# Kernel tuning notes

Hardware: AMD Instinct MI355X
Metric: run time of the kernel (lower is better)

## Reference

```python
import jax, jax.numpy as jnp
import numpy as np
import math

C = 8  # sparsity factor c from __init__


def setup_inputs() -> dict:
    key = jax.random.key(0)
    kq, kk, kv, ki = jax.random.split(key, 4)
    B, Q, KV, D = 4, 2048, 2048, 512
    U = int(Q * math.log(KV))  # 15615 sampled keys, matches torch _sampler
    q = jax.random.normal(kq, (B, Q, D), dtype=jnp.float32)
    k = jax.random.normal(kk, (B, KV, D), dtype=jnp.float32)
    v = jax.random.normal(kv, (B, KV, D), dtype=jnp.float32)
    sample_idx = jax.random.randint(ki, (B, U), 0, KV)  # per-batch random key sample
    return {"q": q, "k": k, "v": v, "sample_idx": sample_idx}


def reference(q, k, v, sample_idx):
    B, Q, D = q.shape
    KV = k.shape[1]
    u = int(C * math.log(Q))  # number of selected queries (== 60 here)

    # _sampler: gather sampled keys per batch -> (B, U, D)
    k_bar = jnp.take_along_axis(k, sample_idx[:, :, None], axis=1)

    # sparsity measure M = max_j s_bar - mean_j s_bar, s_bar: (B, Q, U)
    s_bar = jnp.einsum('bqd,bud->bqu', q, k_bar)
    M = s_bar.max(axis=2) - s_bar.mean(axis=2)  # (B, Q)

    # top-u queries per batch
    _, top_idx = jax.lax.top_k(M, u)  # (B, u)
    q_bar = jnp.take_along_axis(q, top_idx[:, :, None], axis=1)  # (B, u, D)

    # small dense attention over full keys; NOTE: original scales by sqrt(kv_len)
    attn = jnp.einsum('bud,bkd->buk', q_bar, k) / jnp.sqrt(jnp.asarray(KV, q.dtype))
    attn = jax.nn.softmax(attn, axis=-1)
    s1 = jnp.einsum('buk,bkd->bud', attn, v)  # (B, u, D)

    # fill all positions with mean of v, then scatter attention outputs
    s = jnp.broadcast_to(v.mean(axis=1, keepdims=True), q.shape)  # (B, Q, D)
    bidx = jnp.arange(B)[:, None]
    s = s.at[bidx, top_idx].set(s1)
    return s
```

## Files before the change

### kernel.cpp

```cpp
#include <hip/hip_runtime.h>
#include <math.h>

#define BATCH 4
#define QN    2048
#define KVN   2048
#define DN    512
#define U_TOT 15615
#define NSEL  60
#define NSLOT 32
#define S1KS  64

typedef __attribute__((ext_vector_type(8))) short bf16x8;
typedef __attribute__((ext_vector_type(4))) float f32x4;

__device__ __forceinline__ unsigned short f2bf(float f) {
  unsigned u = __float_as_uint(f);
  unsigned r = (u + 0x7fffu + ((u >> 16) & 1u)) >> 16;
  return (unsigned short)r;
}
__device__ __forceinline__ float bf2f(unsigned short h) {
  return __uint_as_float(((unsigned)h) << 16);
}
__device__ __forceinline__ void gld16(const void* g, void* l) {
  __builtin_amdgcn_global_load_lds(
      (const __attribute__((address_space(1))) unsigned int*)g,
      (__attribute__((address_space(3))) unsigned int*)l, 16, 0, 0);
}

__global__ __launch_bounds__(256) void split_kernel(
    const float* __restrict__ q, const float* __restrict__ k,
    unsigned short* __restrict__ qhi, unsigned short* __restrict__ qlo,
    unsigned short* __restrict__ khi, unsigned short* __restrict__ klo)
{
  const int half = blockIdx.x >> 12;
  const int i = (blockIdx.x & 4095) * 256 + threadIdx.x;
  const float* in = half ? k : q;
  unsigned short* hi = half ? khi : qhi;
  unsigned short* lo = half ? klo : qlo;
  float4 f = reinterpret_cast<const float4*>(in)[i];
  ushort4 h, l;
  h.x = f2bf(f.x); l.x = f2bf(f.x - bf2f(h.x));
  h.y = f2bf(f.y); l.y = f2bf(f.y - bf2f(h.y));
  h.z = f2bf(f.z); l.z = f2bf(f.z - bf2f(h.z));
  h.w = f2bf(f.w); l.w = f2bf(f.w - bf2f(h.w));
  reinterpret_cast<ushort4*>(hi)[i] = h;
  reinterpret_cast<ushort4*>(lo)[i] = l;
}

__global__ __launch_bounds__(1024) void count_kernel(
    const int* __restrict__ sidx, float* __restrict__ cnt)
{
  __shared__ int h[KVN];
  const int b = blockIdx.x, t = threadIdx.x;
  for (int i = t; i < KVN; i += 1024) h[i] = 0;
  __syncthreads();
  for (int i = t; i < U_TOT; i += 1024) atomicAdd(&h[sidx[b * U_TOT + i]], 1);
  __syncthreads();
  for (int i = t; i < KVN; i += 1024) cnt[b * KVN + i] = (float)h[i];
}

__global__ __launch_bounds__(256) void s_mfma_kernel(
    const unsigned short* __restrict__ qh, const unsigned short* __restrict__ ql,
    const unsigned short* __restrict__ kh, const unsigned short* __restrict__ kl,
    const float* __restrict__ cnt, float* __restrict__ Pmax, float* __restrict__ Psum)
{
  __shared__ unsigned short Ah[128 * 32];
  __shared__ unsigned short Al[128 * 32];
  __shared__ unsigned short Bh[128 * 32];
  __shared__ unsigned short Bl[128 * 32];
  __shared__ float cnt_s[128];

  const int t = threadIdx.x;
  const int w = t >> 6;
  const int L = t & 63;
  const int mbase = (w & 1) * 64;
  const int nbase = (w >> 1) * 64;
  const int lm = L & 15;

  const int bid = blockIdx.x;
  const int xcd = bid & 7;
  const int idx = bid >> 3;
  const int b   = xcd >> 1;
  const int ji  = (xcd & 1) * 8 + (idx >> 3);
  const int qi0 = (idx & 7) * 2;
  const int j0  = ji * 128;

  if (t < 128) cnt_s[t] = cnt[b * KVN + j0 + t];

  const int srow = t >> 2;
  const int schk = (t & 3) ^ ((t >> 3) & 3);

  const int perm  = (L >> 4) ^ ((lm >> 1) & 3);
  const int abase = (mbase * 4 + lm * 4 + perm) * 8;
  const int bbase = (nbase * 4 + lm * 4 + perm) * 8;

  const size_t koff0 = ((size_t)(b * KVN) + j0 + srow) * DN + (size_t)(schk * 8);
  const size_t koff1 = koff0 + (size_t)64 * DN;

  for (int qq = 0; qq < 2; ++qq) {
    const int q0 = (qi0 + qq) * 128;
    const size_t qoff0 = ((size_t)(b * QN) + q0 + srow) * DN + (size_t)(schk * 8);
    const size_t qoff1 = qoff0 + (size_t)64 * DN;

    f32x4 acc[4][4];
#pragma unroll
    for (int nf = 0; nf < 4; ++nf)
#pragma unroll
      for (int mf = 0; mf < 4; ++mf) {
        acc[nf][mf][0] = 0.f; acc[nf][mf][1] = 0.f;
        acc[nf][mf][2] = 0.f; acc[nf][mf][3] = 0.f;
      }

    for (int d0 = 0; d0 < DN; d0 += 32) {
      __syncthreads();
      gld16(qh + qoff0 + d0, &Ah[t * 8]);
      gld16(qh + qoff1 + d0, &Ah[(t + 256) * 8]);
      gld16(ql + qoff0 + d0, &Al[t * 8]);
      gld16(ql + qoff1 + d0, &Al[(t + 256) * 8]);
      gld16(kh + koff0 + d0, &Bh[t * 8]);
      gld16(kh + koff1 + d0, &Bh[(t + 256) * 8]);
      gld16(kl + koff0 + d0, &Bl[t * 8]);
      gld16(kl + koff1 + d0, &Bl[(t + 256) * 8]);
      __syncthreads();

      bf16x8 ah[4], al[4];
#pragma unroll
      for (int mf = 0; mf < 4; ++mf) {
        ah[mf] = *reinterpret_cast<const bf16x8*>(&Ah[abase + mf * 512]);
        al[mf] = *reinterpret_cast<const bf16x8*>(&Al[abase + mf * 512]);
      }
#pragma unroll
      for (int nf = 0; nf < 4; ++nf) {
        bf16x8 bh = *reinterpret_cast<const bf16x8*>(&Bh[bbase + nf * 512]);
        bf16x8 bl = *reinterpret_cast<const bf16x8*>(&Bl[bbase + nf * 512]);
#pragma unroll
        for (int mf = 0; mf < 4; ++mf) {
          acc[nf][mf] = __builtin_amdgcn_mfma_f32_16x16x32_bf16(ah[mf], bh, acc[nf][mf], 0, 0, 0);
          acc[nf][mf] = __builtin_amdgcn_mfma_f32_16x16x32_bf16(ah[mf], bl, acc[nf][mf], 0, 0, 0);
          acc[nf][mf] = __builtin_amdgcn_mfma_f32_16x16x32_bf16(al[mf], bh, acc[nf][mf], 0, 0, 0);
        }
      }
    }

    float mx[4][4], wsm[4][4];
#pragma unroll
    for (int mf = 0; mf < 4; ++mf)
#pragma unroll
      for (int r = 0; r < 4; ++r) { mx[mf][r] = -INFINITY; wsm[mf][r] = 0.f; }

#pragma unroll
    for (int nf = 0; nf < 4; ++nf) {
      const float c = cnt_s[nbase + nf * 16 + lm];
      const bool has = (c > 0.f);
#pragma unroll
      for (int mf = 0; mf < 4; ++mf)
#pragma unroll
        for (int r = 0; r < 4; ++r) {
          const float v = acc[nf][mf][r];
          if (has) mx[mf][r] = fmaxf(mx[mf][r], v);
          wsm[mf][r] = fmaf(c, v, wsm[mf][r]);
        }
    }

    const size_t spi = (size_t)((ji * 2 + (w >> 1)) * BATCH + b);
#pragma unroll
    for (int mf = 0; mf < 4; ++mf)
#pragma unroll
      for (int r = 0; r < 4; ++r) {
        float m = mx[mf][r], s = wsm[mf][r];
#pragma unroll
        for (int o = 1; o < 16; o <<= 1) {
          m = fmaxf(m, __shfl_xor(m, o));
          s += __shfl_xor(s, o);
        }
        if (lm == 0) {
          const int qrow = q0 + mbase + mf * 16 + (L >> 4) * 4 + r;
          Pmax[spi * QN + qrow] = m;
          Psum[spi * QN + qrow] = s;
        }
      }
  }
}

__global__ __launch_bounds__(256) void combine_kernel(
    const float* __restrict__ Pmax, const float* __restrict__ Psum, float* __restrict__ M)
{
  const int g = blockIdx.x * 256 + threadIdx.x;
  const int b = g >> 11;
  const int qq = g & (QN - 1);
  float m = -INFINITY, s = 0.f;
#pragma unroll 4
  for (int p = 0; p < NSLOT; ++p) {
    m = fmaxf(m, Pmax[((size_t)(p * BATCH + b)) * QN + qq]);
    s += Psum[((size_t)(p * BATCH + b)) * QN + qq];
  }
  M[g] = m - s * (1.0f / (float)U_TOT);
}

__global__ __launch_bounds__(256) void select_kernel(
    const float* __restrict__ M, int* __restrict__ topidx, int* __restrict__ rowslot)
{
  const int b = blockIdx.x;
  const int t = threadIdx.x;
  unsigned long long key[8];
#pragma unroll
  for (int s = 0; s < 8; ++s) {
    const int qq = s * 256 + t;
    unsigned u = __float_as_uint(M[b * QN + qq]);
    u = (u & 0x80000000u) ? ~u : (u | 0x80000000u);
    key[s] = ((unsigned long long)u << 32) | (unsigned)(QN - qq);
    rowslot[b * QN + qq] = -1;
  }

  __shared__ unsigned hist[256];
  __shared__ unsigned long long pref_s;
  __shared__ unsigned rank_s;
  __shared__ unsigned cnt_s;
  if (t == 0) { pref_s = 0ull; rank_s = NSEL; cnt_s = 0u; }
  __syncthreads();

  for (int level = 7; level >= 0; --level) {
    const int shift = level * 8;
    hist[t] = 0;
    __syncthreads();
    const unsigned long long pref = pref_s;
    const unsigned rank = rank_s;
#pragma unroll
    for (int s = 0; s < 8; ++s) {
      const bool match = (level == 7) || ((key[s] >> (shift + 8)) == pref);
      if (match) atomicAdd(&hist[(unsigned)((key[s] >> shift) & 255u)], 1u);
    }
    __syncthreads();
    if (t < 64) {
      const unsigned h0 = hist[4 * t], h1 = hist[4 * t + 1];
      const unsigned h2 = hist[4 * t + 2], h3 = hist[4 * t + 3];
      const unsigned loc = h0 + h1 + h2 + h3;
      unsigned run = loc;
#pragma unroll
      for (int o = 1; o < 64; o <<= 1) {
        const unsigned oth = (unsigned)__shfl_down((int)run, o);
        if (t + o < 64) run += oth;
      }
      const unsigned suf = run - loc;
      const unsigned c3 = suf, c2 = c3 + h3, c1 = c2 + h2, c0 = c1 + h1;
      int hit = -1; unsigned cgt = 0;
      if      (c3 < rank && rank <= c3 + h3) { hit = 4 * t + 3; cgt = c3; }
      else if (c2 < rank && rank <= c2 + h2) { hit = 4 * t + 2; cgt = c2; }
      else if (c1 < rank && rank <= c1 + h1) { hit = 4 * t + 1; cgt = c1; }
      else if (c0 < rank && rank <= c0 + h0) { hit = 4 * t + 0; cgt = c0; }
      if (hit >= 0) {
        pref_s = ((level == 7) ? 0ull : (pref_s << 8)) | (unsigned long long)(unsigned)hit;
        rank_s = rank - cgt;
      }
    }
    __syncthreads();
  }

  const unsigned long long T = pref_s;
#pragma unroll
  for (int s = 0; s < 8; ++s) {
    if (key[s] >= T) {
      const unsigned pos = atomicAdd(&cnt_s, 1u);
      const int qsel = QN - (int)(key[s] & 0xFFFFFFFFull);
      topidx[b * 64 + pos] = qsel;
      rowslot[b * QN + qsel] = (int)pos;
    }
  }
}

#define SBM 64
#define SBN 32
#define SBK 32
__global__ __launch_bounds__(256) void scores_kernel(
    const float* __restrict__ q, const int* __restrict__ topidx,
    const float* __restrict__ k, float* __restrict__ attn)
{
  __shared__ float a_s[SBK][SBM + 4];
  __shared__ float b_s[SBK][SBN + 4];
  __shared__ int tix_s[64];
  const int t  = threadIdx.x;
  const int tx = t & 7;
  const int ty = t >> 3;
  const int kv0 = blockIdx.x * SBN;
  const int b   = blockIdx.y;
  const float* kb = k + (size_t)b * KVN * DN;

  if (t < 64) tix_s[t] = (t < NSEL) ? topidx[b * 64 + t] : 0;
  __syncthreads();

  float acc[2][4];
#pragma unroll
  for (int i = 0; i < 2; ++i)
#pragma unroll
    for (int j = 0; j < 4; ++j) acc[i][j] = 0.f;

  const int c4 = (t & 7) * 4;
  const int r0 = t >> 3;
  const int srow0 = tix_s[r0];
  const int srow1 = tix_s[r0 + 32];

  for (int d0 = 0; d0 < DN; d0 += SBK) {
#pragma unroll
    for (int rr = 0; rr < 2; ++rr) {
      int row = r0 + rr * 32;
      int srow = rr ? srow1 : srow0;
      float4 av = *reinterpret_cast<const float4*>(q + ((size_t)(b * QN) + srow) * DN + d0 + c4);
      a_s[c4 + 0][row] = av.x; a_s[c4 + 1][row] = av.y;
      a_s[c4 + 2][row] = av.z; a_s[c4 + 3][row] = av.w;
    }
    {
      float4 bv = *reinterpret_cast<const float4*>(kb + (size_t)(kv0 + r0) * DN + d0 + c4);
      b_s[c4 + 0][r0] = bv.x; b_s[c4 + 1][r0] = bv.y;
      b_s[c4 + 2][r0] = bv.z; b_s[c4 + 3][r0] = bv.w;
    }
    __syncthreads();
#pragma unroll
    for (int kk = 0; kk < SBK; ++kk) {
      const float a0 = a_s[kk][ty * 2];
      const float a1 = a_s[kk][ty * 2 + 1];
      float4 bv = *reinterpret_cast<const float4*>(&b_s[kk][tx * 4]);
      float bf[4] = {bv.x, bv.y, bv.z, bv.w};
#pragma unroll
      for (int j = 0; j < 4; ++j) {
        acc[0][j] = fmaf(a0, bf[j], acc[0][j]);
        acc[1][j] = fmaf(a1, bf[j], acc[1][j]);
      }
    }
    __syncthreads();
  }

#pragma unroll
  for (int i = 0; i < 2; ++i) {
    int j = ty * 2 + i;
    if (j < NSEL) {
      float4 o = make_float4(acc[i][0], acc[i][1], acc[i][2], acc[i][3]);
      *reinterpret_cast<float4*>(attn + ((size_t)(b * NSEL + j)) * KVN + kv0 + tx * 4) = o;
    }
  }
}

__global__ __launch_bounds__(256) void softmax_kernel(float* __restrict__ attn)
{
  __shared__ float buf[KVN];
  __shared__ float red[256];
  const int t = threadIdx.x;
  float* row = attn + (size_t)blockIdx.x * KVN;

  float m = -INFINITY;
  for (int i = t; i < KVN; i += 256) { float v = row[i]; buf[i] = v; m = fmaxf(m, v); }
  red[t] = m;
  __syncthreads();
  for (int off = 128; off > 0; off >>= 1) {
    if (t < off) red[t] = fmaxf(red[t], red[t + off]);
    __syncthreads();
  }
  m = red[0];
  __syncthreads();

  const float sc = 0.022097086912079608f;
  float s = 0.f;
  for (int i = t; i < KVN; i += 256) { float e = __expf((buf[i] - m) * sc); buf[i] = e; s += e; }
  red[t] = s;
  __syncthreads();
  for (int off = 128; off > 0; off >>= 1) {
    if (t < off) red[t] += red[t + off];
    __syncthreads();
  }
  float inv = 1.f / red[0];
  for (int i = t; i < KVN; i += 256) row[i] = buf[i] * inv;
}

__global__ __launch_bounds__(256) void s1_partial_kernel(
    const float* __restrict__ attn, const float* __restrict__ v,
    float* __restrict__ part, float* __restrict__ vpart)
{
  __shared__ float a_s[32][61];
  const int t    = threadIdx.x;
  const int dv4  = t & 63;
  const int jg   = t >> 6;
  const int dh   = blockIdx.x;
  const int b    = blockIdx.y;
  const int ks   = blockIdx.z;
  const int kv0  = ks * 32;
  const int dbase = dh * 256 + dv4 * 4;

  for (int x = t; x < NSEL * 32; x += 256) {
    const int j = x >> 5, kk = x & 31;
    a_s[kk][j] = attn[((size_t)(b * NSEL + j)) * KVN + kv0 + kk];
  }
  __syncthreads();

  f32x4 acc[15];
#pragma unroll
  for (int i = 0; i < 15; ++i) { acc[i][0] = 0.f; acc[i][1] = 0.f; acc[i][2] = 0.f; acc[i][3] = 0.f; }
  f32x4 vsum; vsum[0] = 0.f; vsum[1] = 0.f; vsum[2] = 0.f; vsum[3] = 0.f;

  const float* vb = v + ((size_t)b * KVN + kv0) * DN + dbase;
#pragma unroll 8
  for (int kk = 0; kk < 32; ++kk) {
    const f32x4 vv = *reinterpret_cast<const f32x4*>(vb + (size_t)kk * DN);
    if (jg == 0) { vsum[0] += vv[0]; vsum[1] += vv[1]; vsum[2] += vv[2]; vsum[3] += vv[3]; }
#pragma unroll
    for (int jj = 0; jj < 15; ++jj) {
      const float a = a_s[kk][jg * 15 + jj];
      acc[jj][0] = fmaf(a, vv[0], acc[jj][0]);
      acc[jj][1] = fmaf(a, vv[1], acc[jj][1]);
      acc[jj][2] = fmaf(a, vv[2], acc[jj][2]);
      acc[jj][3] = fmaf(a, vv[3], acc[jj][3]);
    }
  }

#pragma unroll
  for (int jj = 0; jj < 15; ++jj) {
    const int j = jg * 15 + jj;
    *reinterpret_cast<f32x4*>(
        part + ((size_t)((ks * BATCH + b) * NSEL) + j) * DN + dbase) = acc[jj];
  }
  if (jg == 0)
    *reinterpret_cast<f32x4*>(vpart + ((size_t)(ks * BATCH + b)) * DN + dbase) = vsum;
}

__global__ void vmean_combine_kernel(const float* __restrict__ vpart, float* __restrict__ vmean)
{
  int idx = blockIdx.x * 256 + threadIdx.x;
  if (idx < BATCH * DN) {
    int b = idx / DN, d = idx % DN;
    float s = 0.f;
    for (int c = 0; c < S1KS; ++c) s += vpart[(size_t)(c * BATCH + b) * DN + d];
    vmean[idx] = s * (1.0f / (float)KVN);
  }
}

__global__ __launch_bounds__(256) void out_kernel(
    const float* __restrict__ part, const float* __restrict__ vmean,
    const int* __restrict__ rowslot, float* __restrict__ out)
{
  const int gid = blockIdx.x * 256 + threadIdx.x;
  const int d4 = gid & 127;
  const int qq = (gid >> 7) & (QN - 1);
  const int b  = gid >> 18;
  const int slot = rowslot[b * QN + qq];
  f32x4 o;
  if (slot >= 0) {
    o[0] = 0.f; o[1] = 0.f; o[2] = 0.f; o[3] = 0.f;
    for (int ks = 0; ks < S1KS; ++ks) {
      const f32x4 p = reinterpret_cast<const f32x4*>(part)[
          ((size_t)((ks * BATCH + b) * NSEL) + slot) * (DN / 4) + d4];
      o[0] += p[0]; o[1] += p[1]; o[2] += p[2]; o[3] += p[3];
    }
  } else {
    o = reinterpret_cast<const f32x4*>(vmean)[b * (DN / 4) + d4];
  }
  reinterpret_cast<f32x4*>(out)[gid] = o;
}

extern "C" void kernel_launch(void* const* d_in, const int* in_sizes, int n_in,
                              void* d_out, int out_size, void* d_ws, size_t ws_size,
                              hipStream_t stream) {
  const float* q    = (const float*)d_in[0];
  const float* k    = (const float*)d_in[1];
  const float* v    = (const float*)d_in[2];
  const int*   sidx = (const int*)d_in[3];
  float* out = (float*)d_out;
  char*  W   = (char*)d_ws;

  const size_t NEL = (size_t)BATCH * QN * DN;
  unsigned short* qh = (unsigned short*)W;
  unsigned short* ql = qh + NEL;
  unsigned short* kh = ql + NEL;
  unsigned short* kl = kh + NEL;

  char* W2 = W + 37748736;
  float* cnt     = (float*)W2;
  float* Pmax    = (float*)(W2 + 32768);
  float* Psum    = (float*)(W2 + 32768 + 1048576);
  float* Mbuf    = (float*)(W2 + 32768 + 2097152);
  int*   topidx  = (int*)(W2 + 32768 + 2097152 + 32768);
  int*   rowslot = (int*)(W2 + 32768 + 2097152 + 32768 + 4096);

  float* attn  = (float*)W;
  float* part  = (float*)(W + 2097152);
  float* vpart = (float*)(W + 33554432);
  float* vmean = (float*)(W + 34078720);

  split_kernel<<<dim3(8192), 256, 0, stream>>>(q, k, qh, ql, kh, kl);
  count_kernel<<<dim3(BATCH), 1024, 0, stream>>>(sidx, cnt);
  s_mfma_kernel<<<dim3(512), 256, 0, stream>>>(qh, ql, kh, kl, cnt, Pmax, Psum);
  combine_kernel<<<dim3(BATCH * QN / 256), 256, 0, stream>>>(Pmax, Psum, Mbuf);
  select_kernel<<<dim3(BATCH), 256, 0, stream>>>(Mbuf, topidx, rowslot);
  scores_kernel<<<dim3(KVN / SBN, BATCH), 256, 0, stream>>>(q, topidx, k, attn);
  softmax_kernel<<<dim3(BATCH * NSEL), 256, 0, stream>>>(attn);
  s1_partial_kernel<<<dim3(2, BATCH, S1KS), 256, 0, stream>>>(attn, v, part, vpart);
  vmean_combine_kernel<<<dim3(8), 256, 0, stream>>>(vpart, vmean);
  out_kernel<<<dim3(4096), 256, 0, stream>>>(part, vmean, rowslot, out);
}
```

Measured before the change: 233.2 us.

## Fuse prep kernels, fold combine into select, atomic vmean, shuffle softmax reductions

Merges the bf16 split, the key-count histogram (now split across 8 partial blocks per batch), the vmean zeroing and the rowslot init into one prep kernel. The combine pass is folded into select_kernel, and vmean is accumulated with atomics inside s1_partial, which removes the vmean_combine kernel. Softmax reductions switch from LDS tree loops to wave shuffles. Together these cut three kernel launches and several serial phases, at the cost of extra partial-count reads in s_mfma, a serial 32-slot read loop in select's 4 blocks, and nondeterministic float atomic ordering for vmean.

```diff
diff --git a/kernel.cpp b/kernel.cpp
--- a/kernel.cpp
+++ b/kernel.cpp
@@ -9,6 +9,7 @@
 #define NSEL  60
 #define NSLOT 32
 #define S1KS  64
+#define CPART 8
 
 typedef __attribute__((ext_vector_type(8))) short bf16x8;
 typedef __attribute__((ext_vector_type(4))) float f32x4;
@@ -27,42 +28,55 @@
       (__attribute__((address_space(3))) unsigned int*)l, 16, 0, 0);
 }
 
-__global__ __launch_bounds__(256) void split_kernel(
+__global__ __launch_bounds__(256) void prep_kernel(
     const float* __restrict__ q, const float* __restrict__ k,
     unsigned short* __restrict__ qhi, unsigned short* __restrict__ qlo,
-    unsigned short* __restrict__ khi, unsigned short* __restrict__ klo)
-{
-  const int half = blockIdx.x >> 12;
-  const int i = (blockIdx.x & 4095) * 256 + threadIdx.x;
-  const float* in = half ? k : q;
-  unsigned short* hi = half ? khi : qhi;
-  unsigned short* lo = half ? klo : qlo;
-  float4 f = reinterpret_cast<const float4*>(in)[i];
-  ushort4 h, l;
-  h.x = f2bf(f.x); l.x = f2bf(f.x - bf2f(h.x));
-  h.y = f2bf(f.y); l.y = f2bf(f.y - bf2f(h.y));
-  h.z = f2bf(f.z); l.z = f2bf(f.z - bf2f(h.z));
-  h.w = f2bf(f.w); l.w = f2bf(f.w - bf2f(h.w));
-  reinterpret_cast<ushort4*>(hi)[i] = h;
-  reinterpret_cast<ushort4*>(lo)[i] = l;
-}
-
-__global__ __launch_bounds__(1024) void count_kernel(
-    const int* __restrict__ sidx, float* __restrict__ cnt)
+    unsigned short* __restrict__ khi, unsigned short* __restrict__ klo,
+    const int* __restrict__ sidx, float* __restrict__ cntp,
+    float* __restrict__ vmean, int* __restrict__ rowslot)
 {
   __shared__ int h[KVN];
-  const int b = blockIdx.x, t = threadIdx.x;
-  for (int i = t; i < KVN; i += 1024) h[i] = 0;
-  __syncthreads();
-  for (int i = t; i < U_TOT; i += 1024) atomicAdd(&h[sidx[b * U_TOT + i]], 1);
-  __syncthreads();
-  for (int i = t; i < KVN; i += 1024) cnt[b * KVN + i] = (float)h[i];
+  const int bid = blockIdx.x;
+  const int t = threadIdx.x;
+
+  if (bid < 8192) {
+    const int half = bid >> 12;
+    const int i = (bid & 4095) * 256 + t;
+    const float* in = half ? k : q;
+    unsigned short* hi = half ? khi : qhi;
+    unsigned short* lo = half ? klo : qlo;
+    float4 f = reinterpret_cast<const float4*>(in)[i];
+    ushort4 hh, ll;
+    hh.x = f2bf(f.x); ll.x = f2bf(f.x - bf2f(hh.x));
+    hh.y = f2bf(f.y); ll.y = f2bf(f.y - bf2f(hh.y));
+    hh.z = f2bf(f.z); ll.z = f2bf(f.z - bf2f(hh.z));
+    hh.w = f2bf(f.w); ll.w = f2bf(f.w - bf2f(hh.w));
+    reinterpret_cast<ushort4*>(hi)[i] = hh;
+    reinterpret_cast<ushort4*>(lo)[i] = ll;
+  } else if (bid < 8224) {
+    const int cb = bid - 8192;
+    const int b  = cb >> 3;
+    const int p  = cb & 7;
+    for (int i = t; i < KVN; i += 256) h[i] = 0;
+    __syncthreads();
+    const int start = p * 1952;
+    const int end   = (start + 1952 < U_TOT) ? start + 1952 : U_TOT;
+    for (int i = start + t; i < end; i += 256) atomicAdd(&h[sidx[b * U_TOT + i]], 1);
+    __syncthreads();
+    for (int i = t; i < KVN; i += 256)
+      cntp[((size_t)(p * BATCH + b)) * KVN + i] = (float)h[i];
+  } else if (bid == 8224) {
+    for (int i = t; i < BATCH * DN; i += 256) vmean[i] = 0.f;
+  } else {
+    const int idx = (bid - 8225) * 256 + t;
+    rowslot[idx] = -1;
+  }
 }
 
 __global__ __launch_bounds__(256) void s_mfma_kernel(
     const unsigned short* __restrict__ qh, const unsigned short* __restrict__ ql,
     const unsigned short* __restrict__ kh, const unsigned short* __restrict__ kl,
-    const float* __restrict__ cnt, float* __restrict__ Pmax, float* __restrict__ Psum)
+    const float* __restrict__ cntp, float* __restrict__ Pmax, float* __restrict__ Psum)
 {
   __shared__ unsigned short Ah[128 * 32];
   __shared__ unsigned short Al[128 * 32];
@@ -85,7 +99,13 @@
   const int qi0 = (idx & 7) * 2;
   const int j0  = ji * 128;
 
-  if (t < 128) cnt_s[t] = cnt[b * KVN + j0 + t];
+  if (t < 128) {
+    float c = 0.f;
+#pragma unroll
+    for (int p = 0; p < CPART; ++p)
+      c += cntp[((size_t)(p * BATCH + b)) * KVN + j0 + t];
+    cnt_s[t] = c;
+  }
 
   const int srow = t >> 2;
   const int schk = (t & 3) ^ ((t >> 3) & 3);
@@ -182,23 +202,9 @@
   }
 }
 
-__global__ __launch_bounds__(256) void combine_kernel(
-    const float* __restrict__ Pmax, const float* __restrict__ Psum, float* __restrict__ M)
-{
-  const int g = blockIdx.x * 256 + threadIdx.x;
-  const int b = g >> 11;
-  const int qq = g & (QN - 1);
-  float m = -INFINITY, s = 0.f;
-#pragma unroll 4
-  for (int p = 0; p < NSLOT; ++p) {
-    m = fmaxf(m, Pmax[((size_t)(p * BATCH + b)) * QN + qq]);
-    s += Psum[((size_t)(p * BATCH + b)) * QN + qq];
-  }
-  M[g] = m - s * (1.0f / (float)U_TOT);
-}
-
 __global__ __launch_bounds__(256) void select_kernel(
-    const float* __restrict__ M, int* __restrict__ topidx, int* __restrict__ rowslot)
+    const float* __restrict__ Pmax, const float* __restrict__ Psum,
+    int* __restrict__ topidx, int* __restrict__ rowslot)
 {
   const int b = blockIdx.x;
   const int t = threadIdx.x;
@@ -206,10 +212,16 @@
 #pragma unroll
   for (int s = 0; s < 8; ++s) {
     const int qq = s * 256 + t;
-    unsigned u = __float_as_uint(M[b * QN + qq]);
+    float m = -INFINITY, sm = 0.f;
+#pragma unroll 4
+    for (int p = 0; p < NSLOT; ++p) {
+      m = fmaxf(m, Pmax[((size_t)(p * BATCH + b)) * QN + qq]);
+      sm += Psum[((size_t)(p * BATCH + b)) * QN + qq];
+    }
+    const float M = m - sm * (1.0f / (float)U_TOT);
+    unsigned u = __float_as_uint(M);
     u = (u & 0x80000000u) ? ~u : (u | 0x80000000u);
     key[s] = ((unsigned long long)u << 32) | (unsigned)(QN - qq);
-    rowslot[b * QN + qq] = -1;
   }
 
   __shared__ unsigned hist[256];
@@ -342,37 +354,34 @@
 __global__ __launch_bounds__(256) void softmax_kernel(float* __restrict__ attn)
 {
   __shared__ float buf[KVN];
-  __shared__ float red[256];
+  __shared__ float wred[4];
   const int t = threadIdx.x;
+  const int L = t & 63, wv = t >> 6;
   float* row = attn + (size_t)blockIdx.x * KVN;
 
   float m = -INFINITY;
   for (int i = t; i < KVN; i += 256) { float v = row[i]; buf[i] = v; m = fmaxf(m, v); }
-  red[t] = m;
-  __syncthreads();
-  for (int off = 128; off > 0; off >>= 1) {
-    if (t < off) red[t] = fmaxf(red[t], red[t + off]);
-    __syncthreads();
-  }
-  m = red[0];
-  __syncthreads();
+#pragma unroll
+  for (int o = 1; o < 64; o <<= 1) m = fmaxf(m, __shfl_xor(m, o));
+  if (L == 0) wred[wv] = m;
+  __syncthreads();
+  m = fmaxf(fmaxf(wred[0], wred[1]), fmaxf(wred[2], wred[3]));
 
   const float sc = 0.022097086912079608f;
   float s = 0.f;
   for (int i = t; i < KVN; i += 256) { float e = __expf((buf[i] - m) * sc); buf[i] = e; s += e; }
-  red[t] = s;
-  __syncthreads();
-  for (int off = 128; off > 0; off >>= 1) {
-    if (t < off) red[t] += red[t + off];
-    __syncthreads();
-  }
-  float inv = 1.f / red[0];
+#pragma unroll
+  for (int o = 1; o < 64; o <<= 1) s += __shfl_xor(s, o);
+  __syncthreads();
+  if (L == 0) wred[wv] = s;
+  __syncthreads();
+  const float inv = 1.f / (wred[0] + wred[1] + wred[2] + wred[3]);
   for (int i = t; i < KVN; i += 256) row[i] = buf[i] * inv;
 }
 
 __global__ __launch_bounds__(256) void s1_partial_kernel(
     const float* __restrict__ attn, const float* __restrict__ v,
-    float* __restrict__ part, float* __restrict__ vpart)
+    float* __restrict__ part, float* __restrict__ vmean)
 {
   __shared__ float a_s[32][61];
   const int t    = threadIdx.x;
@@ -416,18 +425,12 @@
     *reinterpret_cast<f32x4*>(
         part + ((size_t)((ks * BATCH + b) * NSEL) + j) * DN + dbase) = acc[jj];
   }
-  if (jg == 0)
-    *reinterpret_cast<f32x4*>(vpart + ((size_t)(ks * BATCH + b)) * DN + dbase) = vsum;
-}
-
-__global__ void vmean_combine_kernel(const float* __restrict__ vpart, float* __restrict__ vmean)
-{
-  int idx = blockIdx.x * 256 + threadIdx.x;
-  if (idx < BATCH * DN) {
-    int b = idx / DN, d = idx % DN;
-    float s = 0.f;
-    for (int c = 0; c < S1KS; ++c) s += vpart[(size_t)(c * BATCH + b) * DN + d];
-    vmean[idx] = s * (1.0f / (float)KVN);
+  if (jg == 0) {
+    float* vm = vmean + (size_t)b * DN + dbase;
+    atomicAdd(vm + 0, vsum[0]);
+    atomicAdd(vm + 1, vsum[1]);
+    atomicAdd(vm + 2, vsum[2]);
+    atomicAdd(vm + 3, vsum[3]);
   }
 }
 
@@ -449,7 +452,9 @@
       o[0] += p[0]; o[1] += p[1]; o[2] += p[2]; o[3] += p[3];
     }
   } else {
-    o = reinterpret_cast<const f32x4*>(vmean)[b * (DN / 4) + d4];
+    const f32x4 vm = reinterpret_cast<const f32x4*>(vmean)[b * (DN / 4) + d4];
+    const float sc = 1.0f / (float)KVN;
+    o[0] = vm[0] * sc; o[1] = vm[1] * sc; o[2] = vm[2] * sc; o[3] = vm[3] * sc;
   }
   reinterpret_cast<f32x4*>(out)[gid] = o;
 }
@@ -470,27 +475,22 @@
   unsigned short* kh = ql + NEL;
   unsigned short* kl = kh + NEL;
 
-  char* W2 = W + 37748736;
-  float* cnt     = (float*)W2;
-  float* Pmax    = (float*)(W2 + 32768);
-  float* Psum    = (float*)(W2 + 32768 + 1048576);
-  float* Mbuf    = (float*)(W2 + 32768 + 2097152);
-  int*   topidx  = (int*)(W2 + 32768 + 2097152 + 32768);
-  int*   rowslot = (int*)(W2 + 32768 + 2097152 + 32768 + 4096);
-
   float* attn  = (float*)W;
   float* part  = (float*)(W + 2097152);
-  float* vpart = (float*)(W + 33554432);
   float* vmean = (float*)(W + 34078720);
 
-  split_kernel<<<dim3(8192), 256, 0, stream>>>(q, k, qh, ql, kh, kl);
-  count_kernel<<<dim3(BATCH), 1024, 0, stream>>>(sidx, cnt);
-  s_mfma_kernel<<<dim3(512), 256, 0, stream>>>(qh, ql, kh, kl, cnt, Pmax, Psum);
-  combine_kernel<<<dim3(BATCH * QN / 256), 256, 0, stream>>>(Pmax, Psum, Mbuf);
-  select_kernel<<<dim3(BATCH), 256, 0, stream>>>(Mbuf, topidx, rowslot);
+  char* W2 = W + 37748736;
+  float* cntp    = (float*)W2;
+  float* Pmax    = (float*)(W2 + 262144);
+  float* Psum    = (float*)(W2 + 262144 + 1048576);
+  int*   topidx  = (int*)(W2 + 262144 + 2097152);
+  int*   rowslot = (int*)(W2 + 262144 + 2097152 + 4096);
+
+  prep_kernel<<<dim3(8257), 256, 0, stream>>>(q, k, qh, ql, kh, kl, sidx, cntp, vmean, rowslot);
+  s_mfma_kernel<<<dim3(512), 256, 0, stream>>>(qh, ql, kh, kl, cntp, Pmax, Psum);
+  select_kernel<<<dim3(BATCH), 256, 0, stream>>>(Pmax, Psum, topidx, rowslot);
   scores_kernel<<<dim3(KVN / SBN, BATCH), 256, 0, stream>>>(q, topidx, k, attn);
   softmax_kernel<<<dim3(BATCH * NSEL), 256, 0, stream>>>(attn);
-  s1_partial_kernel<<<dim3(2, BATCH, S1KS), 256, 0, stream>>>(attn, v, part, vpart);
-  vmean_combine_kernel<<<dim3(8), 256, 0, stream>>>(vpart, vmean);
+  s1_partial_kernel<<<dim3(2, BATCH, S1KS), 256, 0, stream>>>(attn, v, part, vmean);
   out_kernel<<<dim3(4096), 256, 0, stream>>>(part, vmean, rowslot, out);
 }
```

Measured after the change: 238.6 us. +2.3%, slower.
